# Kernel optimization log

Hardware: AMD Instinct MI355X
Metric: run time of the kernel (lower is better)

The kernel has to match this reference:

```python
import jax, jax.numpy as jnp
import numpy as np

B, T, V, E, U = 1024, 256, 50000, 512, 1024

def setup_inputs() -> dict:
    key = jax.random.key(0)
    ks = jax.random.split(key, 10)
    s = lambda k, shape, fan: jax.random.normal(k, shape, dtype=jnp.float32) * (1.0 / np.sqrt(fan))
    return {
        "inputs": jax.random.randint(ks[0], (B, T), 0, V, dtype=jnp.int32),
        "emb": s(ks[1], (V, E), E),
        "W0": s(ks[2], (E, U), E),
        "U0": s(ks[3], (U, U), U),
        "b0": jnp.zeros((U,), jnp.float32),
        "W1": s(ks[4], (U, U), U),
        "U1": s(ks[5], (U, U), U),
        "b1": jnp.zeros((U,), jnp.float32),
        "Wout": s(ks[6], (U, 1), U),
        "bout": jnp.zeros((1,), jnp.float32),
    }

def reference(inputs, emb, W0, U0, b0, W1, U1, b1, Wout, bout):
    x = emb[inputs]                      # [B, T, E] embedding lookup
    xT = jnp.swapaxes(x, 0, 1)           # [T, B, E] time-major for scan
    h0_init = jnp.zeros((inputs.shape[0], U0.shape[0]), x.dtype)
    h1_init = jnp.zeros((inputs.shape[0], U1.shape[0]), x.dtype)

    def step(carry, xt):
        h0, h1 = carry
        h0 = jnp.tanh(xt @ W0 + h0 @ U0 + b0)   # SimpleRNNCell 0 (dropout inactive, inference)
        h1 = jnp.tanh(h0 @ W1 + h1 @ U1 + b1)   # SimpleRNNCell 1
        return (h0, h1), None

    (h0, h1), _ = jax.lax.scan(step, (h0_init, h1_init), xT)
    return jax.nn.sigmoid(h1 @ Wout + bout)      # [B, 1]
```

## Files before the change

### kernel.cpp

```cpp
#include <hip/hip_runtime.h>
#include <hip/hip_cooperative_groups.h>
#include <math.h>

namespace cg = cooperative_groups;

typedef unsigned short u16;
typedef __bf16 bf16x8 __attribute__((ext_vector_type(8)));
typedef float f32x4 __attribute__((ext_vector_type(4)));
typedef unsigned short u16x8 __attribute__((ext_vector_type(8)));
typedef int i32x4 __attribute__((ext_vector_type(4)));

#define NBLK 256
#define NTHR 512
#define BB 1024
#define TT 256
#define EE 512
#define UU 1024
#define K0 1536
#define K1 2048
#define NK0 48
#define NK1 64
#define KTL0 32
#define KTL1 16
#define HN0 ((size_t)BB * K0)
#define HN1 ((size_t)BB * K1)
#define LDS_BYTES 163840

#define ROSTER_BASE 0
#define FLAG_BASE 32
#define EPOCH_BASE (32 + 2048)
#define BAR_INTS 2560

#define AUX_SC0 1
#define AUX_L1  0

__device__ i32x4 llvm_amdgcn_raw_buffer_load_i32x4(i32x4 srsrc, int voffset, int soffset,
                                                   int aux) __asm("llvm.amdgcn.raw.buffer.load.v4i32");

__device__ __forceinline__ i32x4 make_srd(const void* p) {
  union { const void* p; int i[2]; } u; u.p = p;
  i32x4 r; r.x = u.i[0]; r.y = u.i[1]; r.z = -1; r.w = 0x00020000;
  return r;
}

__device__ __forceinline__ u16 f2bf(float f) {
  unsigned u = __builtin_bit_cast(unsigned, f);
  u += 0x7fffu + ((u >> 16) & 1u);
  return (u16)(u >> 16);
}
__device__ __forceinline__ float bf2f(u16 h) {
  return __builtin_bit_cast(float, ((unsigned)h) << 16);
}
__device__ __forceinline__ float fast_tanh(float x) {
  x = fminf(fmaxf(x, -15.f), 15.f);
  float e = __expf(2.f * x);
  return (e - 1.f) / (e + 1.f);
}

template<int K, int KLOW>
__device__ __forceinline__ void wfill(u16* __restrict__ Wt,
    const float* __restrict__ Wl, const float* __restrict__ Wh, int gstart) {
  constexpr int NK = K / 32;
  constexpr int NG = 1024 * K / 8;
  for (int g = gstart; g < NG; g += NBLK * NTHR) {
    const int lane = g & 63;
    const int r = g >> 6;
    const int kt = r % NK;
    const int cb = r / NK;
    const int n = cb * 16 + (lane & 15);
    const int kb = kt * 32 + (lane >> 4) * 8;
    u16x8 o;
#pragma unroll
    for (int e = 0; e < 8; ++e) {
      const int k = kb + e;
      const float v = (k < KLOW) ? Wl[(size_t)k * UU + n] : Wh[(size_t)(k - KLOW) * UU + n];
      o[e] = f2bf(v);
    }
    *(u16x8*)(Wt + (size_t)g * 8) = o;
  }
}

__device__ __forceinline__ void xbar(int* __restrict__ bar, int xcc, int slot, int nx,
                                     int tgt, int tid) {
  __syncthreads();
  if (tid < 64) {
    if (tid == 0)
      __hip_atomic_store(&bar[FLAG_BASE + xcc * 256 + slot], tgt,
                         __ATOMIC_RELAXED, __HIP_MEMORY_SCOPE_AGENT);
    if (slot == 0) {
      for (int base = 0; base < nx; base += 64) {
        const int i = base + tid;
        const bool act = (i < nx);
        int guard = 0;
        bool done = false;
        do {
          int v = act ? __hip_atomic_load(&bar[FLAG_BASE + xcc * 256 + i],
                                          __ATOMIC_RELAXED, __HIP_MEMORY_SCOPE_AGENT)
                      : tgt;
          done = __all(v >= tgt) != 0;
        } while (!done && ++guard < 300000);
      }
      if (tid == 0)
        __hip_atomic_store(&bar[EPOCH_BASE + xcc * 32], tgt,
                           __ATOMIC_RELAXED, __HIP_MEMORY_SCOPE_AGENT);
    } else if (tid == 0) {
      int guard = 0;
      while (__hip_atomic_load(&bar[EPOCH_BASE + xcc * 32],
                               __ATOMIC_RELAXED, __HIP_MEMORY_SCOPE_AGENT) < tgt
             && ++guard < 600000)
        __builtin_amdgcn_s_sleep(8);
    }
  }
  __syncthreads();
}

__device__ __forceinline__ void mf1(const i32x4& av,
    const u16* __restrict__ p0, const u16* __restrict__ p1,
    const u16* __restrict__ q2, const u16* __restrict__ q3,
    size_t koff, int lo, f32x4 (&acc)[4]) {
  u16x8 b0 = *(const u16x8*)(p0 + koff + lo);
  u16x8 b1 = *(const u16x8*)(p1 + koff + lo);
  u16x8 b2 = *(const u16x8*)(q2 + koff + lo);
  u16x8 b3 = *(const u16x8*)(q3 + koff + lo);
  bf16x8 fa0 = __builtin_bit_cast(bf16x8, av);
  bf16x8 fb0 = __builtin_bit_cast(bf16x8, b0);
  bf16x8 fb1 = __builtin_bit_cast(bf16x8, b1);
  bf16x8 fb2 = __builtin_bit_cast(bf16x8, b2);
  bf16x8 fb3 = __builtin_bit_cast(bf16x8, b3);
  acc[0] = __builtin_amdgcn_mfma_f32_16x16x32_bf16(fa0, fb0, acc[0], 0, 0, 0);
  acc[1] = __builtin_amdgcn_mfma_f32_16x16x32_bf16(fa0, fb1, acc[1], 0, 0, 0);
  acc[2] = __builtin_amdgcn_mfma_f32_16x16x32_bf16(fa0, fb2, acc[2], 0, 0, 0);
  acc[3] = __builtin_amdgcn_mfma_f32_16x16x32_bf16(fa0, fb3, acc[3], 0, 0, 0);
}

__device__ __forceinline__ void mf1r(const i32x4& av,
    const u16* __restrict__ p0, const u16* __restrict__ p1,
    size_t koff, int lo, const i32x4& b2v, const i32x4& b3v, f32x4 (&acc)[4]) {
  u16x8 b0 = *(const u16x8*)(p0 + koff + lo);
  u16x8 b1 = *(const u16x8*)(p1 + koff + lo);
  bf16x8 fa0 = __builtin_bit_cast(bf16x8, av);
  bf16x8 fb0 = __builtin_bit_cast(bf16x8, b0);
  bf16x8 fb1 = __builtin_bit_cast(bf16x8, b1);
  bf16x8 fb2 = __builtin_bit_cast(bf16x8, b2v);
  bf16x8 fb3 = __builtin_bit_cast(bf16x8, b3v);
  acc[0] = __builtin_amdgcn_mfma_f32_16x16x32_bf16(fa0, fb0, acc[0], 0, 0, 0);
  acc[1] = __builtin_amdgcn_mfma_f32_16x16x32_bf16(fa0, fb1, acc[1], 0, 0, 0);
  acc[2] = __builtin_amdgcn_mfma_f32_16x16x32_bf16(fa0, fb2, acc[2], 0, 0, 0);
  acc[3] = __builtin_amdgcn_mfma_f32_16x16x32_bf16(fa0, fb3, acc[3], 0, 0, 0);
}

template<int K, int KTL>
__device__ __forceinline__ void gemm2(const i32x4& srdA, int voA,
    const u16* __restrict__ bA, const u16* __restrict__ bB,
    const u16* __restrict__ bP, int lane, f32x4 (&acc)[4]) {
  constexpr int NK = K / 32;
  const int lo = lane * 8;

  if constexpr (KTL == 0) {
    const u16* p0 = bA;
    const u16* p1 = bA + (size_t)NK * 512;
    const u16* q2 = bB;
    const u16* q3 = bB + (size_t)NK * 512;
#pragma unroll 8
    for (int kt = 0; kt < NK; ++kt) {
      i32x4 a0 = llvm_amdgcn_raw_buffer_load_i32x4(srdA, voA + kt * 64, 0, AUX_SC0);
      mf1(a0, p0, p1, q2, q3, (size_t)kt * 512, lo, acc);
    }
  } else {
    constexpr int NGP = KTL / 8;
    constexpr int NGS = (NK - KTL) / 4;
    const u16* p0 = bA;
    const u16* p1 = bA + (size_t)NK * 512;
    const u16* bP3 = bP + (size_t)KTL * 512;
    i32x4 srdB = make_srd(bB);
    const int lob = lane * 16;

    i32x4 aE[8], aO[8];
    i32x4 sAE[4], sBE[8], sAO[4], sBO[8];

#pragma unroll
    for (int j = 0; j < 8; ++j)
      aE[j] = llvm_amdgcn_raw_buffer_load_i32x4(srdA, voA + j * 64, 0, AUX_SC0);

#pragma unroll
    for (int g = 0; g < NGP; ++g) {
      if (g + 1 < NGP) {
#pragma unroll
        for (int j = 0; j < 8; ++j) {
          i32x4 v = llvm_amdgcn_raw_buffer_load_i32x4(srdA, voA + ((g + 1) * 8 + j) * 64, 0, AUX_SC0);
          if ((g & 1) == 0) aO[j] = v; else aE[j] = v;
        }
      } else {
#pragma unroll
        for (int j = 0; j < 4; ++j) {
          sAE[j] = llvm_amdgcn_raw_buffer_load_i32x4(srdA, voA + (KTL + j) * 64, 0, AUX_SC0);
          sBE[2 * j]     = llvm_amdgcn_raw_buffer_load_i32x4(srdB, (0 * NK + KTL + j) * 1024 + lob, 0, AUX_L1);
          sBE[2 * j + 1] = llvm_amdgcn_raw_buffer_load_i32x4(srdB, (1 * NK + KTL + j) * 1024 + lob, 0, AUX_L1);
        }
      }
      __builtin_amdgcn_sched_barrier(0);
#pragma unroll
      for (int j = 0; j < 8; ++j) {
        const int kt = g * 8 + j;
        if ((g & 1) == 0) mf1(aE[j], p0, p1, bP, bP3, (size_t)kt * 512, lo, acc);
        else              mf1(aO[j], p0, p1, bP, bP3, (size_t)kt * 512, lo, acc);
      }
      __builtin_amdgcn_sched_barrier(0);
    }

#pragma unroll
    for (int s = 0; s < NGS; ++s) {
      if (s + 1 < NGS) {
        const int kb = KTL + (s + 1) * 4;
#pragma unroll
        for (int j = 0; j < 4; ++j) {
          i32x4 va = llvm_amdgcn_raw_buffer_load_i32x4(srdA, voA + (kb + j) * 64, 0, AUX_SC0);
          i32x4 v2 = llvm_amdgcn_raw_buffer_load_i32x4(srdB, (0 * NK + kb + j) * 1024 + lob, 0, AUX_L1);
          i32x4 v3 = llvm_amdgcn_raw_buffer_load_i32x4(srdB, (1 * NK + kb + j) * 1024 + lob, 0, AUX_L1);
          if ((s & 1) == 0) { sAO[j] = va; sBO[2 * j] = v2; sBO[2 * j + 1] = v3; }
          else              { sAE[j] = va; sBE[2 * j] = v2; sBE[2 * j + 1] = v3; }
        }
      }
      __builtin_amdgcn_sched_barrier(0);
#pragma unroll
      for (int j = 0; j < 4; ++j) {
        const int kt = KTL + s * 4 + j;
        if ((s & 1) == 0) mf1r(sAE[j], p0, p1, (size_t)kt * 512, lo, sBE[2 * j], sBE[2 * j + 1], acc);
        else              mf1r(sAO[j], p0, p1, (size_t)kt * 512, lo, sBO[2 * j], sBO[2 * j + 1], acc);
      }
      __builtin_amdgcn_sched_barrier(0);
    }
  }
}

__device__ __forceinline__ void do_l0(int tk, int xcc, int jl, bool uselds,
    const u16* __restrict__ ldsb, const u16* __restrict__ Wt0,
    const int* __restrict__ inputs, const float* __restrict__ emb,
    const float* __restrict__ b0, u16* __restrict__ A0, u16* __restrict__ A1,
    int tid)
{
  const int lane = tid & 63, w = tid >> 6, q = lane >> 4, l16 = lane & 15;
  const int c0 = jl * 64;
  if (tk < TT - 1) {
    const int grow = xcc * 128 + jl * 8 + (tid >> 6);
    const int c = (tid & 63) * 8;
    const int idx = inputs[grow * TT + tk + 1];
    const f32x4* s = (const f32x4*)(emb + (size_t)idx * EE + c);
    f32x4 f0 = s[0], f1 = s[1];
    u16x8 oa;
#pragma unroll
    for (int j = 0; j < 4; ++j) { oa[j] = f2bf(f0[j]); oa[j + 4] = f2bf(f1[j]); }
    *(u16x8*)(A0 + (size_t)((tk + 1) & 1) * HN0 + (size_t)grow * K0 + c) = oa;
  }
  if (tk < TT) {
    f32x4 acc[4];
#pragma unroll
    for (int n = 0; n < 4; ++n) acc[n] = (f32x4){0.f, 0.f, 0.f, 0.f};
    i32x4 srdA = make_srd(A0 + (size_t)(tk & 1) * HN0);
    const int voA = ((xcc * 128 + w * 16 + l16) * K0 + q * 8) * 2;
    const u16* gA = Wt0 + (size_t)(c0 / 16) * NK0 * 512;
    const u16* bB = Wt0 + (size_t)(c0 / 16 + 2) * NK0 * 512;
    if (uselds) gemm2<K0, KTL0>(srdA, voA, ldsb, bB,
                                ldsb + (size_t)2 * NK0 * 512, lane, acc);
    else        gemm2<K0, 0   >(srdA, voA, gA, bB, ldsb, lane, acc);
    u16* d1 = A1 + (size_t)(tk & 1) * HN1;
    u16* d2 = A0 + (size_t)((tk + 1) & 1) * HN0 + 512;
#pragma unroll
    for (int n = 0; n < 4; ++n) {
      const int col = c0 + n * 16 + l16;
      const float bs = b0[col];
#pragma unroll
      for (int rr = 0; rr < 4; ++rr) {
        const int grow = xcc * 128 + w * 16 + q * 4 + rr;
        const u16 v = f2bf(fast_tanh(acc[n][rr] + bs));
        d1[(size_t)grow * K1 + col] = v;
        d2[(size_t)grow * K0 + col] = v;
      }
    }
  }
}

__device__ __forceinline__ void do_l1(int tk, int xcc, int jl, bool uselds,
    const u16* __restrict__ ldsb, const u16* __restrict__ Wt1,
    const float* __restrict__ b1, u16* __restrict__ A1, int tid)
{
  const int lane = tid & 63, w = tid >> 6, q = lane >> 4, l16 = lane & 15;
  const int c0 = jl * 64;
  f32x4 acc[4];
#pragma unroll
  for (int n = 0; n < 4; ++n) acc[n] = (f32x4){0.f, 0.f, 0.f, 0.f};
  i32x4 srdA = make_srd(A1 + (size_t)((tk - 1) & 1) * HN1);
  const int voA = ((xcc * 128 + w * 16 + l16) * K1 + q * 8) * 2;
  const u16* gA = Wt1 + (size_t)(c0 / 16) * NK1 * 512;
  const u16* bB = Wt1 + (size_t)(c0 / 16 + 2) * NK1 * 512;
  if (uselds) gemm2<K1, KTL1>(srdA, voA, ldsb, bB,
                              ldsb + (size_t)2 * NK1 * 512, lane, acc);
  else        gemm2<K1, 0   >(srdA, voA, gA, bB, ldsb, lane, acc);
  u16* d1 = A1 + (size_t)(tk & 1) * HN1 + 1024;
#pragma unroll
  for (int n = 0; n < 4; ++n) {
    const int col = c0 + n * 16 + l16;
    const float bs = b1[col];
#pragma unroll
    for (int rr = 0; rr < 4; ++rr) {
      const int grow = xcc * 128 + w * 16 + q * 4 + rr;
      d1[(size_t)grow * K1 + col] = f2bf(fast_tanh(acc[n][rr] + bs));
    }
  }
}

__global__ __launch_bounds__(NTHR, 2)
void rnn_kernel(const int* __restrict__ inputs, const float* __restrict__ emb,
    const float* __restrict__ W0, const float* __restrict__ U0, const float* __restrict__ b0,
    const float* __restrict__ W1, const float* __restrict__ U1, const float* __restrict__ b1,
    const float* __restrict__ Wout, const float* __restrict__ bout,
    float* __restrict__ out,
    u16* __restrict__ Wt0, u16* __restrict__ Wt1,
    u16* __restrict__ A0, u16* __restrict__ A1, int* __restrict__ bar)
{
  extern __shared__ u16 lds[];
  int* li = (int*)lds;
  cg::grid_group grid = cg::this_grid();
  const int tid = threadIdx.x, bid = blockIdx.x;

  const int gstart = bid * NTHR + tid;
  wfill<K0, 512>(Wt0, W0, U0, gstart);
  wfill<K1, 1024>(Wt1, W1, U1, gstart);
  for (int g = gstart; g < BB * EE / 8; g += NBLK * NTHR) {
    const int b = g >> 6, seg = g & 63;
    const int idx = inputs[b * TT];
    const f32x4* s = (const f32x4*)(emb + (size_t)idx * EE + seg * 8);
    f32x4 f0 = s[0], f1 = s[1];
    u16x8 o;
#pragma unroll
    for (int j = 0; j < 4; ++j) { o[j] = f2bf(f0[j]); o[j + 4] = f2bf(f1[j]); }
    *(u16x8*)(A0 + (size_t)b * K0 + seg * 8) = o;
  }
  {
    const u16x8 z = {0, 0, 0, 0, 0, 0, 0, 0};
    for (int g = gstart; g < BB * 1024 / 8; g += NBLK * NTHR) {
      const int b = g >> 7, seg = g & 127;
      *(u16x8*)(A0 + (size_t)b * K0 + 512 + seg * 8) = z;
      *(u16x8*)(A1 + (size_t)b * K1 + 1024 + seg * 8) = z;
    }
  }
  if (bid == 0) for (int i = tid; i < BAR_INTS; i += NTHR) bar[i] = 0;
  grid.sync();

  if (tid == 0) {
    const int xc = __builtin_amdgcn_s_getreg((7 << 11) | 20) & 7;
    li[0] = xc;
    li[1] = atomicAdd(&bar[ROSTER_BASE + xc], 1);
  }
  __syncthreads();
  const int xcc = li[0], slot = li[1];
  __syncthreads();
  grid.sync();
  if (tid == 0)
    li[0] = __hip_atomic_load(&bar[ROSTER_BASE + xcc],
                              __ATOMIC_RELAXED, __HIP_MEMORY_SCOPE_AGENT);
  __syncthreads();
  const int nx = li[0];
  __syncthreads();

  if (slot < 32) {
    const bool pL0 = slot < 16;
    const int cb = (pL0 ? slot : slot - 16) * 4;
    const int NKp = pL0 ? NK0 : NK1;
    const int KTLp = pL0 ? KTL0 : KTL1;
    const u16* W = pL0 ? Wt0 : Wt1;
    const u16x8* s = (const u16x8*)(W + (size_t)cb * NKp * 512);
    const int nv = 2 * NKp * 64;
    u16x8* d = (u16x8*)lds;
    for (int i = tid; i < nv; i += NTHR) d[i] = s[i];
    u16x8* d2 = d + nv;
    const int nv2 = 2 * KTLp * 64;
    for (int i = tid; i < nv2; i += NTHR) {
      const int f = i / (KTLp * 64);
      const int rem = i - f * (KTLp * 64);
      d2[i] = *((const u16x8*)(W + (size_t)(cb + 2 + f) * NKp * 512) + rem);
    }
  }
  __syncthreads();

  for (int tk = 0; tk <= TT; ++tk) {
    for (int job = slot; job < 32; job += nx) {
      const bool uselds = (job == slot);
      if (job < 16) do_l0(tk, xcc, job, uselds, lds, Wt0, inputs, emb, b0, A0, A1, tid);
      else if (tk >= 1) do_l1(tk, xcc, job - 16, uselds, lds, Wt1, b1, A1, tid);
    }
    xbar(bar, xcc, slot, nx, tk + 1, tid);
  }

  if (slot == 0) {
    const int lane = tid & 63, w = tid >> 6;
    i32x4 srdH = make_srd(A1);
    const f32x4* wv = (const f32x4*)(Wout + lane * 16);
    f32x4 w0 = wv[0], w1 = wv[1], w2 = wv[2], w3 = wv[3];
    for (int rr = 0; rr < 16; ++rr) {
      const int grow = xcc * 128 + w * 16 + rr;
      const int vo = (grow * K1 + 1024 + lane * 16) * 2;
      i32x4 hv0 = llvm_amdgcn_raw_buffer_load_i32x4(srdH, vo, 0, AUX_SC0);
      i32x4 hv1 = llvm_amdgcn_raw_buffer_load_i32x4(srdH, vo + 16, 0, AUX_SC0);
      u16x8 lo = __builtin_bit_cast(u16x8, hv0);
      u16x8 hi = __builtin_bit_cast(u16x8, hv1);
      float s = 0.f;
#pragma unroll
      for (int j = 0; j < 4; ++j) {
        s += bf2f(lo[j]) * w0[j];
        s += bf2f(lo[j + 4]) * w1[j];
        s += bf2f(hi[j]) * w2[j];
        s += bf2f(hi[j + 4]) * w3[j];
      }
#pragma unroll
      for (int off = 32; off > 0; off >>= 1) s += __shfl_down(s, off);
      if (lane == 0) out[grow] = 1.f / (1.f + expf(-(s + bout[0])));
    }
  }
}

extern "C" void kernel_launch(void* const* d_in, const int* in_sizes, int n_in,
                              void* d_out, int out_size, void* d_ws, size_t ws_size,
                              hipStream_t stream)
{
  (void)in_sizes; (void)n_in; (void)out_size; (void)ws_size;
  const int*   inputs = (const int*)d_in[0];
  const float* emb    = (const float*)d_in[1];
  const float* W0     = (const float*)d_in[2];
  const float* U0     = (const float*)d_in[3];
  const float* b0     = (const float*)d_in[4];
  const float* W1     = (const float*)d_in[5];
  const float* U1     = (const float*)d_in[6];
  const float* b1     = (const float*)d_in[7];
  const float* Wout   = (const float*)d_in[8];
  const float* bout   = (const float*)d_in[9];
  float* out = (float*)d_out;

  u16* Wt0 = (u16*)d_ws;
  u16* Wt1 = Wt0 + (size_t)1024 * K0;
  u16* A0  = Wt1 + (size_t)1024 * K1;
  u16* A1  = A0 + (size_t)2 * 1024 * K0;
  int* bar = (int*)(A1 + (size_t)2 * 1024 * K1);

  static int lds_set = 0;
  if (!lds_set) {
    hipFuncSetAttribute((const void*)rnn_kernel,
                        hipFuncAttributeMaxDynamicSharedMemorySize, LDS_BYTES);
    lds_set = 1;
  }

  void* args[] = { &inputs, &emb, &W0, &U0, &b0, &W1, &U1, &b1, &Wout, &bout,
                   &out, &Wt0, &Wt1, &A0, &A1, &bar };
  hipLaunchCooperativeKernel((void*)rnn_kernel, dim3(NBLK), dim3(NTHR), args, LDS_BYTES, stream);
}
```

Measured before the change: 6.028 ms.

## Double block threads and split each wave's output columns across two wave groups

Doubles threads per block from 512 to 1024 and splits each 64-column job's four 16-column MFMA tiles between two wave halves, so each wave computes two tiles instead of four. The LDS-resident path is split too: one half reads both column tiles from LDS, the other streams the partly LDS / partly global second pair. This roughly halves per-wave serial MFMA work per timestep and adds waves per CU to hide latency. In exchange each wave reloads the A operand, doubling A traffic, and register budget per thread tightens under the larger launch bound.

```diff
diff --git a/kernel.cpp b/kernel.cpp
--- a/kernel.cpp
+++ b/kernel.cpp
@@ -8,10 +8,11 @@
 typedef __bf16 bf16x8 __attribute__((ext_vector_type(8)));
 typedef float f32x4 __attribute__((ext_vector_type(4)));
 typedef unsigned short u16x8 __attribute__((ext_vector_type(8)));
+typedef unsigned short u16x4 __attribute__((ext_vector_type(4)));
 typedef int i32x4 __attribute__((ext_vector_type(4)));
 
 #define NBLK 256
-#define NTHR 512
+#define NTHR 1024
 #define BB 1024
 #define TT 256
 #define EE 512
@@ -114,122 +115,134 @@
   __syncthreads();
 }
 
-__device__ __forceinline__ void mf1(const i32x4& av,
+__device__ __forceinline__ void mf2(const i32x4& av,
     const u16* __restrict__ p0, const u16* __restrict__ p1,
-    const u16* __restrict__ q2, const u16* __restrict__ q3,
-    size_t koff, int lo, f32x4 (&acc)[4]) {
-  u16x8 b0 = *(const u16x8*)(p0 + koff + lo);
-  u16x8 b1 = *(const u16x8*)(p1 + koff + lo);
-  u16x8 b2 = *(const u16x8*)(q2 + koff + lo);
-  u16x8 b3 = *(const u16x8*)(q3 + koff + lo);
-  bf16x8 fa0 = __builtin_bit_cast(bf16x8, av);
-  bf16x8 fb0 = __builtin_bit_cast(bf16x8, b0);
-  bf16x8 fb1 = __builtin_bit_cast(bf16x8, b1);
-  bf16x8 fb2 = __builtin_bit_cast(bf16x8, b2);
-  bf16x8 fb3 = __builtin_bit_cast(bf16x8, b3);
-  acc[0] = __builtin_amdgcn_mfma_f32_16x16x32_bf16(fa0, fb0, acc[0], 0, 0, 0);
-  acc[1] = __builtin_amdgcn_mfma_f32_16x16x32_bf16(fa0, fb1, acc[1], 0, 0, 0);
-  acc[2] = __builtin_amdgcn_mfma_f32_16x16x32_bf16(fa0, fb2, acc[2], 0, 0, 0);
-  acc[3] = __builtin_amdgcn_mfma_f32_16x16x32_bf16(fa0, fb3, acc[3], 0, 0, 0);
-}
-
-__device__ __forceinline__ void mf1r(const i32x4& av,
-    const u16* __restrict__ p0, const u16* __restrict__ p1,
-    size_t koff, int lo, const i32x4& b2v, const i32x4& b3v, f32x4 (&acc)[4]) {
+    size_t koff, int lo, f32x4 (&acc)[2]) {
   u16x8 b0 = *(const u16x8*)(p0 + koff + lo);
   u16x8 b1 = *(const u16x8*)(p1 + koff + lo);
   bf16x8 fa0 = __builtin_bit_cast(bf16x8, av);
   bf16x8 fb0 = __builtin_bit_cast(bf16x8, b0);
   bf16x8 fb1 = __builtin_bit_cast(bf16x8, b1);
-  bf16x8 fb2 = __builtin_bit_cast(bf16x8, b2v);
-  bf16x8 fb3 = __builtin_bit_cast(bf16x8, b3v);
   acc[0] = __builtin_amdgcn_mfma_f32_16x16x32_bf16(fa0, fb0, acc[0], 0, 0, 0);
   acc[1] = __builtin_amdgcn_mfma_f32_16x16x32_bf16(fa0, fb1, acc[1], 0, 0, 0);
-  acc[2] = __builtin_amdgcn_mfma_f32_16x16x32_bf16(fa0, fb2, acc[2], 0, 0, 0);
-  acc[3] = __builtin_amdgcn_mfma_f32_16x16x32_bf16(fa0, fb3, acc[3], 0, 0, 0);
+}
+
+__device__ __forceinline__ void mf2r(const i32x4& av,
+    const i32x4& b0v, const i32x4& b1v, f32x4 (&acc)[2]) {
+  bf16x8 fa0 = __builtin_bit_cast(bf16x8, av);
+  bf16x8 fb0 = __builtin_bit_cast(bf16x8, b0v);
+  bf16x8 fb1 = __builtin_bit_cast(bf16x8, b1v);
+  acc[0] = __builtin_amdgcn_mfma_f32_16x16x32_bf16(fa0, fb0, acc[0], 0, 0, 0);
+  acc[1] = __builtin_amdgcn_mfma_f32_16x16x32_bf16(fa0, fb1, acc[1], 0, 0, 0);
+}
+
+template<int K>
+__device__ __forceinline__ void gemmA(const i32x4& srdA, int voA,
+    const u16* __restrict__ bA, int lane, f32x4 (&acc)[2]) {
+  constexpr int NK = K / 32;
+  constexpr int NG = NK / 8;
+  const int lo = lane * 8;
+  const u16* p0 = bA;
+  const u16* p1 = bA + (size_t)NK * 512;
+  i32x4 aE[8], aO[8];
+#pragma unroll
+  for (int j = 0; j < 8; ++j)
+    aE[j] = llvm_amdgcn_raw_buffer_load_i32x4(srdA, voA + j * 64, 0, AUX_SC0);
+#pragma unroll
+  for (int g = 0; g < NG; ++g) {
+    if (g + 1 < NG) {
+#pragma unroll
+      for (int j = 0; j < 8; ++j) {
+        i32x4 v = llvm_amdgcn_raw_buffer_load_i32x4(srdA, voA + ((g + 1) * 8 + j) * 64, 0, AUX_SC0);
+        if ((g & 1) == 0) aO[j] = v; else aE[j] = v;
+      }
+    }
+    __builtin_amdgcn_sched_barrier(0);
+#pragma unroll
+    for (int j = 0; j < 8; ++j) {
+      const int kt = g * 8 + j;
+      if ((g & 1) == 0) mf2(aE[j], p0, p1, (size_t)kt * 512, lo, acc);
+      else              mf2(aO[j], p0, p1, (size_t)kt * 512, lo, acc);
+    }
+    __builtin_amdgcn_sched_barrier(0);
+  }
 }
 
 template<int K, int KTL>
-__device__ __forceinline__ void gemm2(const i32x4& srdA, int voA,
-    const u16* __restrict__ bA, const u16* __restrict__ bB,
-    const u16* __restrict__ bP, int lane, f32x4 (&acc)[4]) {
+__device__ __forceinline__ void gemmB(const i32x4& srdA, int voA,
+    const u16* __restrict__ bP, const u16* __restrict__ gB2, int lane,
+    f32x4 (&acc)[2]) {
+  constexpr int NK = K / 32;
+  constexpr int NGP = KTL / 8;
+  constexpr int NGS = (NK - KTL) / 4;
+  const int lo = lane * 8;
+  const int lob = lane * 16;
+  const u16* p0 = bP;
+  const u16* p1 = bP + (size_t)KTL * 512;
+  i32x4 srdB = make_srd(gB2);
+  i32x4 aE[8], aO[8];
+  i32x4 sAE[4], sBE[8], sAO[4], sBO[8];
+#pragma unroll
+  for (int j = 0; j < 8; ++j)
+    aE[j] = llvm_amdgcn_raw_buffer_load_i32x4(srdA, voA + j * 64, 0, AUX_SC0);
+#pragma unroll
+  for (int g = 0; g < NGP; ++g) {
+    if (g + 1 < NGP) {
+#pragma unroll
+      for (int j = 0; j < 8; ++j) {
+        i32x4 v = llvm_amdgcn_raw_buffer_load_i32x4(srdA, voA + ((g + 1) * 8 + j) * 64, 0, AUX_SC0);
+        if ((g & 1) == 0) aO[j] = v; else aE[j] = v;
+      }
+    } else {
+#pragma unroll
+      for (int j = 0; j < 4; ++j) {
+        sAE[j] = llvm_amdgcn_raw_buffer_load_i32x4(srdA, voA + (KTL + j) * 64, 0, AUX_SC0);
+        sBE[2 * j]     = llvm_amdgcn_raw_buffer_load_i32x4(srdB, (0 * NK + KTL + j) * 1024 + lob, 0, AUX_L1);
+        sBE[2 * j + 1] = llvm_amdgcn_raw_buffer_load_i32x4(srdB, (1 * NK + KTL + j) * 1024 + lob, 0, AUX_L1);
+      }
+    }
+    __builtin_amdgcn_sched_barrier(0);
+#pragma unroll
+    for (int j = 0; j < 8; ++j) {
+      const int kt = g * 8 + j;
+      if ((g & 1) == 0) mf2(aE[j], p0, p1, (size_t)kt * 512, lo, acc);
+      else              mf2(aO[j], p0, p1, (size_t)kt * 512, lo, acc);
+    }
+    __builtin_amdgcn_sched_barrier(0);
+  }
+#pragma unroll
+  for (int s = 0; s < NGS; ++s) {
+    if (s + 1 < NGS) {
+      const int kb = KTL + (s + 1) * 4;
+#pragma unroll
+      for (int j = 0; j < 4; ++j) {
+        i32x4 va = llvm_amdgcn_raw_buffer_load_i32x4(srdA, voA + (kb + j) * 64, 0, AUX_SC0);
+        i32x4 v0 = llvm_amdgcn_raw_buffer_load_i32x4(srdB, (0 * NK + kb + j) * 1024 + lob, 0, AUX_L1);
+        i32x4 v1 = llvm_amdgcn_raw_buffer_load_i32x4(srdB, (1 * NK + kb + j) * 1024 + lob, 0, AUX_L1);
+        if ((s & 1) == 0) { sAO[j] = va; sBO[2 * j] = v0; sBO[2 * j + 1] = v1; }
+        else              { sAE[j] = va; sBE[2 * j] = v0; sBE[2 * j + 1] = v1; }
+      }
+    }
+    __builtin_amdgcn_sched_barrier(0);
+#pragma unroll
+    for (int j = 0; j < 4; ++j) {
+      if ((s & 1) == 0) mf2r(sAE[j], sBE[2 * j], sBE[2 * j + 1], acc);
+      else              mf2r(sAO[j], sBO[2 * j], sBO[2 * j + 1], acc);
+    }
+    __builtin_amdgcn_sched_barrier(0);
+  }
+}
+
+template<int K>
+__device__ __forceinline__ void gemmF(const i32x4& srdA, int voA,
+    const u16* __restrict__ q0, const u16* __restrict__ q1, int lane,
+    f32x4 (&acc)[2]) {
   constexpr int NK = K / 32;
   const int lo = lane * 8;
-
-  if constexpr (KTL == 0) {
-    const u16* p0 = bA;
-    const u16* p1 = bA + (size_t)NK * 512;
-    const u16* q2 = bB;
-    const u16* q3 = bB + (size_t)NK * 512;
 #pragma unroll 8
-    for (int kt = 0; kt < NK; ++kt) {
-      i32x4 a0 = llvm_amdgcn_raw_buffer_load_i32x4(srdA, voA + kt * 64, 0, AUX_SC0);
-      mf1(a0, p0, p1, q2, q3, (size_t)kt * 512, lo, acc);
-    }
-  } else {
-    constexpr int NGP = KTL / 8;
-    constexpr int NGS = (NK - KTL) / 4;
-    const u16* p0 = bA;
-    const u16* p1 = bA + (size_t)NK * 512;
-    const u16* bP3 = bP + (size_t)KTL * 512;
-    i32x4 srdB = make_srd(bB);
-    const int lob = lane * 16;
-
-    i32x4 aE[8], aO[8];
-    i32x4 sAE[4], sBE[8], sAO[4], sBO[8];
-
-#pragma unroll
-    for (int j = 0; j < 8; ++j)
-      aE[j] = llvm_amdgcn_raw_buffer_load_i32x4(srdA, voA + j * 64, 0, AUX_SC0);
-
-#pragma unroll
-    for (int g = 0; g < NGP; ++g) {
-      if (g + 1 < NGP) {
-#pragma unroll
-        for (int j = 0; j < 8; ++j) {
-          i32x4 v = llvm_amdgcn_raw_buffer_load_i32x4(srdA, voA + ((g + 1) * 8 + j) * 64, 0, AUX_SC0);
-          if ((g & 1) == 0) aO[j] = v; else aE[j] = v;
-        }
-      } else {
-#pragma unroll
-        for (int j = 0; j < 4; ++j) {
-          sAE[j] = llvm_amdgcn_raw_buffer_load_i32x4(srdA, voA + (KTL + j) * 64, 0, AUX_SC0);
-          sBE[2 * j]     = llvm_amdgcn_raw_buffer_load_i32x4(srdB, (0 * NK + KTL + j) * 1024 + lob, 0, AUX_L1);
-          sBE[2 * j + 1] = llvm_amdgcn_raw_buffer_load_i32x4(srdB, (1 * NK + KTL + j) * 1024 + lob, 0, AUX_L1);
-        }
-      }
-      __builtin_amdgcn_sched_barrier(0);
-#pragma unroll
-      for (int j = 0; j < 8; ++j) {
-        const int kt = g * 8 + j;
-        if ((g & 1) == 0) mf1(aE[j], p0, p1, bP, bP3, (size_t)kt * 512, lo, acc);
-        else              mf1(aO[j], p0, p1, bP, bP3, (size_t)kt * 512, lo, acc);
-      }
-      __builtin_amdgcn_sched_barrier(0);
-    }
-
-#pragma unroll
-    for (int s = 0; s < NGS; ++s) {
-      if (s + 1 < NGS) {
-        const int kb = KTL + (s + 1) * 4;
-#pragma unroll
-        for (int j = 0; j < 4; ++j) {
-          i32x4 va = llvm_amdgcn_raw_buffer_load_i32x4(srdA, voA + (kb + j) * 64, 0, AUX_SC0);
-          i32x4 v2 = llvm_amdgcn_raw_buffer_load_i32x4(srdB, (0 * NK + kb + j) * 1024 + lob, 0, AUX_L1);
-          i32x4 v3 = llvm_amdgcn_raw_buffer_load_i32x4(srdB, (1 * NK + kb + j) * 1024 + lob, 0, AUX_L1);
-          if ((s & 1) == 0) { sAO[j] = va; sBO[2 * j] = v2; sBO[2 * j + 1] = v3; }
-          else              { sAE[j] = va; sBE[2 * j] = v2; sBE[2 * j + 1] = v3; }
-        }
-      }
-      __builtin_amdgcn_sched_barrier(0);
-#pragma unroll
-      for (int j = 0; j < 4; ++j) {
-        const int kt = KTL + s * 4 + j;
-        if ((s & 1) == 0) mf1r(sAE[j], p0, p1, (size_t)kt * 512, lo, sBE[2 * j], sBE[2 * j + 1], acc);
-        else              mf1r(sAO[j], p0, p1, (size_t)kt * 512, lo, sBO[2 * j], sBO[2 * j + 1], acc);
-      }
-      __builtin_amdgcn_sched_barrier(0);
-    }
+  for (int kt = 0; kt < NK; ++kt) {
+    i32x4 a0 = llvm_amdgcn_raw_buffer_load_i32x4(srdA, voA + kt * 64, 0, AUX_SC0);
+    mf2(a0, q0, q1, (size_t)kt * 512, lo, acc);
   }
 }
 
@@ -239,39 +252,44 @@
     const float* __restrict__ b0, u16* __restrict__ A0, u16* __restrict__ A1,
     int tid)
 {
-  const int lane = tid & 63, w = tid >> 6, q = lane >> 4, l16 = lane & 15;
+  const int lane = tid & 63, wv = tid >> 6, q = lane >> 4, l16 = lane & 15;
+  const int ch = (wv >> 2) & 1;
+  const int rg = (wv & 3) + ((wv >> 3) << 2);
   const int c0 = jl * 64;
   if (tk < TT - 1) {
-    const int grow = xcc * 128 + jl * 8 + (tid >> 6);
-    const int c = (tid & 63) * 8;
+    const int grow = xcc * 128 + jl * 8 + (tid >> 7);
+    const int c = (tid & 127) * 4;
     const int idx = inputs[grow * TT + tk + 1];
-    const f32x4* s = (const f32x4*)(emb + (size_t)idx * EE + c);
-    f32x4 f0 = s[0], f1 = s[1];
-    u16x8 oa;
-#pragma unroll
-    for (int j = 0; j < 4; ++j) { oa[j] = f2bf(f0[j]); oa[j + 4] = f2bf(f1[j]); }
-    *(u16x8*)(A0 + (size_t)((tk + 1) & 1) * HN0 + (size_t)grow * K0 + c) = oa;
+    f32x4 f0 = *(const f32x4*)(emb + (size_t)idx * EE + c);
+    u16x4 oa;
+#pragma unroll
+    for (int j = 0; j < 4; ++j) oa[j] = f2bf(f0[j]);
+    *(u16x4*)(A0 + (size_t)((tk + 1) & 1) * HN0 + (size_t)grow * K0 + c) = oa;
   }
   if (tk < TT) {
-    f32x4 acc[4];
-#pragma unroll
-    for (int n = 0; n < 4; ++n) acc[n] = (f32x4){0.f, 0.f, 0.f, 0.f};
+    f32x4 acc[2];
+#pragma unroll
+    for (int n = 0; n < 2; ++n) acc[n] = (f32x4){0.f, 0.f, 0.f, 0.f};
     i32x4 srdA = make_srd(A0 + (size_t)(tk & 1) * HN0);
-    const int voA = ((xcc * 128 + w * 16 + l16) * K0 + q * 8) * 2;
-    const u16* gA = Wt0 + (size_t)(c0 / 16) * NK0 * 512;
-    const u16* bB = Wt0 + (size_t)(c0 / 16 + 2) * NK0 * 512;
-    if (uselds) gemm2<K0, KTL0>(srdA, voA, ldsb, bB,
-                                ldsb + (size_t)2 * NK0 * 512, lane, acc);
-    else        gemm2<K0, 0   >(srdA, voA, gA, bB, ldsb, lane, acc);
+    const int voA = ((xcc * 128 + rg * 16 + l16) * K0 + q * 8) * 2;
+    const u16* gB = Wt0 + (size_t)(c0 / 16) * NK0 * 512;
+    if (uselds) {
+      if (ch == 0) gemmA<K0>(srdA, voA, ldsb, lane, acc);
+      else         gemmB<K0, KTL0>(srdA, voA, ldsb + (size_t)2 * NK0 * 512,
+                                   Wt0 + (size_t)(c0 / 16 + 2) * NK0 * 512, lane, acc);
+    } else {
+      gemmF<K0>(srdA, voA, gB + (size_t)(ch * 2) * NK0 * 512,
+                gB + (size_t)(ch * 2 + 1) * NK0 * 512, lane, acc);
+    }
     u16* d1 = A1 + (size_t)(tk & 1) * HN1;
     u16* d2 = A0 + (size_t)((tk + 1) & 1) * HN0 + 512;
 #pragma unroll
-    for (int n = 0; n < 4; ++n) {
-      const int col = c0 + n * 16 + l16;
+    for (int n = 0; n < 2; ++n) {
+      const int col = c0 + (ch * 2 + n) * 16 + l16;
       const float bs = b0[col];
 #pragma unroll
       for (int rr = 0; rr < 4; ++rr) {
-        const int grow = xcc * 128 + w * 16 + q * 4 + rr;
+        const int grow = xcc * 128 + rg * 16 + q * 4 + rr;
         const u16 v = f2bf(fast_tanh(acc[n][rr] + bs));
         d1[(size_t)grow * K1 + col] = v;
         d2[(size_t)grow * K0 + col] = v;
@@ -284,32 +302,38 @@
     const u16* __restrict__ ldsb, const u16* __restrict__ Wt1,
     const float* __restrict__ b1, u16* __restrict__ A1, int tid)
 {
-  const int lane = tid & 63, w = tid >> 6, q = lane >> 4, l16 = lane & 15;
+  const int lane = tid & 63, wv = tid >> 6, q = lane >> 4, l16 = lane & 15;
+  const int ch = (wv >> 2) & 1;
+  const int rg = (wv & 3) + ((wv >> 3) << 2);
   const int c0 = jl * 64;
-  f32x4 acc[4];
-#pragma unroll
-  for (int n = 0; n < 4; ++n) acc[n] = (f32x4){0.f, 0.f, 0.f, 0.f};
+  f32x4 acc[2];
+#pragma unroll
+  for (int n = 0; n < 2; ++n) acc[n] = (f32x4){0.f, 0.f, 0.f, 0.f};
   i32x4 srdA = make_srd(A1 + (size_t)((tk - 1) & 1) * HN1);
-  const int voA = ((xcc * 128 + w * 16 + l16) * K1 + q * 8) * 2;
-  const u16* gA = Wt1 + (size_t)(c0 / 16) * NK1 * 512;
-  const u16* bB = Wt1 + (size_t)(c0 / 16 + 2) * NK1 * 512;
-  if (uselds) gemm2<K1, KTL1>(srdA, voA, ldsb, bB,
-                              ldsb + (size_t)2 * NK1 * 512, lane, acc);
-  else        gemm2<K1, 0   >(srdA, voA, gA, bB, ldsb, lane, acc);
+  const int voA = ((xcc * 128 + rg * 16 + l16) * K1 + q * 8) * 2;
+  const u16* gB = Wt1 + (size_t)(c0 / 16) * NK1 * 512;
+  if (uselds) {
+    if (ch == 0) gemmA<K1>(srdA, voA, ldsb, lane, acc);
+    else         gemmB<K1, KTL1>(srdA, voA, ldsb + (size_t)2 * NK1 * 512,
+                                 Wt1 + (size_t)(c0 / 16 + 2) * NK1 * 512, lane, acc);
+  } else {
+    gemmF<K1>(srdA, voA, gB + (size_t)(ch * 2) * NK1 * 512,
+              gB + (size_t)(ch * 2 + 1) * NK1 * 512, lane, acc);
+  }
   u16* d1 = A1 + (size_t)(tk & 1) * HN1 + 1024;
 #pragma unroll
-  for (int n = 0; n < 4; ++n) {
-    const int col = c0 + n * 16 + l16;
+  for (int n = 0; n < 2; ++n) {
+    const int col = c0 + (ch * 2 + n) * 16 + l16;
     const float bs = b1[col];
 #pragma unroll
     for (int rr = 0; rr < 4; ++rr) {
-      const int grow = xcc * 128 + w * 16 + q * 4 + rr;
+      const int grow = xcc * 128 + rg * 16 + q * 4 + rr;
       d1[(size_t)grow * K1 + col] = f2bf(fast_tanh(acc[n][rr] + bs));
     }
   }
 }
 
-__global__ __launch_bounds__(NTHR, 2)
+__global__ __launch_bounds__(NTHR, 4)
 void rnn_kernel(const int* __restrict__ inputs, const float* __restrict__ emb,
     const float* __restrict__ W0, const float* __restrict__ U0, const float* __restrict__ b0,
     const float* __restrict__ W1, const float* __restrict__ U1, const float* __restrict__ b1,
@@ -394,27 +418,29 @@
 
   if (slot == 0) {
     const int lane = tid & 63, w = tid >> 6;
-    i32x4 srdH = make_srd(A1);
-    const f32x4* wv = (const f32x4*)(Wout + lane * 16);
-    f32x4 w0 = wv[0], w1 = wv[1], w2 = wv[2], w3 = wv[3];
-    for (int rr = 0; rr < 16; ++rr) {
-      const int grow = xcc * 128 + w * 16 + rr;
-      const int vo = (grow * K1 + 1024 + lane * 16) * 2;
-      i32x4 hv0 = llvm_amdgcn_raw_buffer_load_i32x4(srdH, vo, 0, AUX_SC0);
-      i32x4 hv1 = llvm_amdgcn_raw_buffer_load_i32x4(srdH, vo + 16, 0, AUX_SC0);
-      u16x8 lo = __builtin_bit_cast(u16x8, hv0);
-      u16x8 hi = __builtin_bit_cast(u16x8, hv1);
-      float s = 0.f;
-#pragma unroll
-      for (int j = 0; j < 4; ++j) {
-        s += bf2f(lo[j]) * w0[j];
-        s += bf2f(lo[j + 4]) * w1[j];
-        s += bf2f(hi[j]) * w2[j];
-        s += bf2f(hi[j + 4]) * w3[j];
-      }
-#pragma unroll
-      for (int off = 32; off > 0; off >>= 1) s += __shfl_down(s, off);
-      if (lane == 0) out[grow] = 1.f / (1.f + expf(-(s + bout[0])));
+    if (w < 8) {
+      i32x4 srdH = make_srd(A1);
+      const f32x4* wv = (const f32x4*)(Wout + lane * 16);
+      f32x4 w0 = wv[0], w1 = wv[1], w2 = wv[2], w3 = wv[3];
+      for (int rr = 0; rr < 16; ++rr) {
+        const int grow = xcc * 128 + w * 16 + rr;
+        const int vo = (grow * K1 + 1024 + lane * 16) * 2;
+        i32x4 hv0 = llvm_amdgcn_raw_buffer_load_i32x4(srdH, vo, 0, AUX_SC0);
+        i32x4 hv1 = llvm_amdgcn_raw_buffer_load_i32x4(srdH, vo + 16, 0, AUX_SC0);
+        u16x8 lo = __builtin_bit_cast(u16x8, hv0);
+        u16x8 hi = __builtin_bit_cast(u16x8, hv1);
+        float s = 0.f;
+#pragma unroll
+        for (int j = 0; j < 4; ++j) {
+          s += bf2f(lo[j]) * w0[j];
+          s += bf2f(lo[j + 4]) * w1[j];
+          s += bf2f(hi[j]) * w2[j];
+          s += bf2f(hi[j + 4]) * w3[j];
+        }
+#pragma unroll
+        for (int off = 32; off > 0; off >>= 1) s += __shfl_down(s, off);
+        if (lane == 0) out[grow] = 1.f / (1.f + expf(-(s + bout[0])));
+      }
     }
   }
 }
```

Result: slower. 9.454 ms (+56.8%).
